# Kernel optimization log

Hardware: AMD Instinct MI355X
Metric: run time of the kernel (lower is better)

## Reference

```python
import jax, jax.numpy as jnp
import numpy as np

NUM_STATES = 2048
NUM_SYMBOLS = 512
SEQ_LEN = 8192


def setup_inputs() -> dict:
    key = jax.random.key(0)
    k_obs, k_A, k_B, k_pi = jax.random.split(key, 4)
    observations = jax.random.randint(k_obs, (SEQ_LEN,), 0, NUM_SYMBOLS, dtype=jnp.int32)
    # Row-stochastic transition matrix A, emission matrix B, initial dist pi
    A = jax.random.uniform(k_A, (NUM_STATES, NUM_STATES), dtype=jnp.float32)
    A = A / A.sum(axis=1, keepdims=True)
    B = jax.random.uniform(k_B, (NUM_STATES, NUM_SYMBOLS), dtype=jnp.float32)
    B = B / B.sum(axis=1, keepdims=True)
    pi = jax.random.uniform(k_pi, (NUM_STATES,), dtype=jnp.float32)
    pi = pi / pi.sum()
    return {"observations": observations, "A": A, "B": B, "pi": pi}


def reference(observations, A, B, pi):
    # Emission likelihoods per timestep: em[t, s] = B[s, o_t]  -> [T, S]
    em = B[:, observations].T
    alpha0 = pi * em[0]                      # [S]

    def step(alpha_prev, em_t):
        alpha_t = (alpha_prev @ A) * em_t    # vector-matrix + elementwise
        return alpha_t, alpha_t

    _, alpha_rest = jax.lax.scan(step, alpha0, em[1:])
    alpha = jnp.concatenate([alpha0[None, :], alpha_rest], axis=0)  # [T, S]
    return alpha
```

## Files before the change

kernel.cpp:

```cpp
#include <hip/hip_runtime.h>


#define S     2048
#define T     8192
#define NSYM  512
#define NBLK  64
#define NTHR  1024
#define READY 0x40000000

typedef int v4i __attribute__((ext_vector_type(4)));

__device__ __forceinline__ v4i load_coherent_i4(const int* p) {
    v4i r;
    asm volatile("global_load_dwordx4 %0, %1, off sc0 sc1\n\ts_waitcnt vmcnt(0)"
                 : "=v"(r) : "v"(p) : "memory");
    return r;
}
__device__ __forceinline__ void store_coherent_i4(int* p, v4i v) {
    asm volatile("global_store_dwordx4 %0, %1, off sc0 sc1"
                 :: "v"(p), "v"(v) : "memory");
}

#define POLL4(e0,e1,e2,e3,bp)                                              \
    asm volatile("global_load_dword %0, %4, off sc0 sc1\n\t"               \
                 "global_load_dword %1, %4, off offset:32 sc0 sc1\n\t"     \
                 "global_load_dword %2, %4, off offset:64 sc0 sc1\n\t"     \
                 "global_load_dword %3, %4, off offset:96 sc0 sc1"         \
                 : "=&v"(e0), "=&v"(e1), "=&v"(e2), "=&v"(e3)              \
                 : "v"(bp) : "memory")

__global__ void __launch_bounds__(NTHR) hmm_fwd(
    const int*   __restrict__ obs,
    const float* __restrict__ A,
    const float* __restrict__ B,
    const float* __restrict__ pi,
    float*       __restrict__ out,
    unsigned*    __restrict__ flag)
{
    __shared__ float4 s_wpart[16][8];
    __shared__ int    s_nz[4];

    const int tx   = threadIdx.x;
    const int b    = blockIdx.x;
    const int lane = tx & 63;
    const int w    = tx >> 6;
    const int jl4  = lane & 7;
    const int r_l  = lane >> 3;
    const int col4 = b * 8 + jl4;
    const float4* A4 = (const float4*)A;

    float4 a_reg[4][4];
    #pragma unroll
    for (int q = 0; q < 4; ++q)
        #pragma unroll
        for (int s = 0; s < 4; ++s) {
            const int i = (w + 16 * q) * 32 + s * 8 + r_l;
            a_reg[q][s] = A4[(size_t)i * (S / 4) + col4];
        }

    if (tx < 8) {
        const int o0 = obs[0];
        const int j  = b * 32 + tx * 4;
        v4i e;
        e.x = __float_as_int(pi[j + 0] * B[(size_t)(j + 0) * NSYM + o0]) + READY;
        e.y = __float_as_int(pi[j + 1] * B[(size_t)(j + 1) * NSYM + o0]) + READY;
        e.z = __float_as_int(pi[j + 2] * B[(size_t)(j + 2) * NSYM + o0]) + READY;
        e.w = __float_as_int(pi[j + 3] * B[(size_t)(j + 3) * NSYM + o0]) + READY;
        store_coherent_i4((int*)out + j, e);
    }
    if (tx == 0) { s_nz[0] = 0; s_nz[1] = 0; s_nz[2] = 0; s_nz[3] = 0; }
    __syncthreads();

    int lastRow = T - 1;

    for (int t = 1; t < T; ++t) {
        float em0 = 0.f, em1 = 0.f, em2 = 0.f, em3 = 0.f;
        if (tx < 8) {
            const int o = obs[t];
            const int j = b * 32 + tx * 4;
            em0 = B[(size_t)(j + 0) * NSYM + o];
            em1 = B[(size_t)(j + 1) * NSYM + o];
            em2 = B[(size_t)(j + 2) * NSYM + o];
            em3 = B[(size_t)(j + 3) * NSYM + o];
        }

        const int* rb = (const int*)(out + (size_t)(t - 1) * S) + r_l;
        const int* b0 = rb + (w +  0) * 32;
        const int* b1 = rb + (w + 16) * 32;
        const int* b2 = rb + (w + 32) * 32;
        const int* b3 = rb + (w + 48) * 32;
        int e00, e01, e02, e03, e10, e11, e12, e13;
        int e20, e21, e22, e23, e30, e31, e32, e33;
        for (;;) {
            POLL4(e00, e01, e02, e03, b0);
            POLL4(e10, e11, e12, e13, b1);
            POLL4(e20, e21, e22, e23, b2);
            POLL4(e30, e31, e32, e33, b3);
            asm volatile("s_waitcnt vmcnt(0)" ::: "memory");
            const int m0 = (e00 < READY) | (e01 < READY) | (e02 < READY) | (e03 < READY);
            const int m1 = (e10 < READY) | (e11 < READY) | (e12 < READY) | (e13 < READY);
            const int m2 = (e20 < READY) | (e21 < READY) | (e22 < READY) | (e23 < READY);
            const int m3 = (e30 < READY) | (e31 < READY) | (e32 < READY) | (e33 < READY);
            if (!(m0 | m1 | m2 | m3)) break;
        }

        float4 acc = make_float4(0.f, 0.f, 0.f, 0.f);
        int nzacc = 0;
        #define STEP1(E, Q, Ss)                                                \
            { const int d = (E) - READY; nzacc |= d;                           \
              const float af = __int_as_float(d);                              \
              acc.x = fmaf(af, a_reg[Q][Ss].x, acc.x);                         \
              acc.y = fmaf(af, a_reg[Q][Ss].y, acc.y);                         \
              acc.z = fmaf(af, a_reg[Q][Ss].z, acc.z);                         \
              acc.w = fmaf(af, a_reg[Q][Ss].w, acc.w); }
        STEP1(e00,0,0) STEP1(e01,0,1) STEP1(e02,0,2) STEP1(e03,0,3)
        STEP1(e10,1,0) STEP1(e11,1,1) STEP1(e12,1,2) STEP1(e13,1,3)
        STEP1(e20,2,0) STEP1(e21,2,1) STEP1(e22,2,2) STEP1(e23,2,3)
        STEP1(e30,3,0) STEP1(e31,3,1) STEP1(e32,3,2) STEP1(e33,3,3)
        #undef STEP1

        #pragma unroll
        for (int m = 8; m <= 32; m <<= 1) {
            acc.x += __shfl_xor(acc.x, m);
            acc.y += __shfl_xor(acc.y, m);
            acc.z += __shfl_xor(acc.z, m);
            acc.w += __shfl_xor(acc.w, m);
        }
        if (lane < 8) s_wpart[w][lane] = acc;
        const unsigned long long nzm = __ballot(nzacc != 0);
        if (nzm != 0ull && lane == 0) s_nz[t & 3] = 1;
        if (tx == 0) s_nz[(t + 2) & 3] = 0;
        __syncthreads();

        if (s_nz[t & 3] == 0) { lastRow = t - 1; break; }

        if (tx < 64) {
            const int h = tx >> 3, c = tx & 7;
            float4 p = s_wpart[h][c];
            const float4 q4 = s_wpart[h + 8][c];
            p.x += q4.x; p.y += q4.y; p.z += q4.z; p.w += q4.w;
            #pragma unroll
            for (int m = 8; m <= 32; m <<= 1) {
                p.x += __shfl_xor(p.x, m);
                p.y += __shfl_xor(p.y, m);
                p.z += __shfl_xor(p.z, m);
                p.w += __shfl_xor(p.w, m);
            }
            if (tx < 8) {
                v4i e;
                e.x = __float_as_int(p.x * em0) + READY;
                e.y = __float_as_int(p.y * em1) + READY;
                e.z = __float_as_int(p.z * em2) + READY;
                e.w = __float_as_int(p.w * em3) + READY;
                store_coherent_i4((int*)(out + (size_t)t * S) + b * 32 + tx * 4, e);
            }
        }
    }

    if (tx == 0)
        __hip_atomic_store(&flag[b], 1u, __ATOMIC_RELAXED, __HIP_MEMORY_SCOPE_AGENT);
    if (tx < 64) {
        for (;;) {
            const unsigned f = __hip_atomic_load(&flag[tx], __ATOMIC_RELAXED,
                                                 __HIP_MEMORY_SCOPE_AGENT);
            if (__all(f == 1u)) break;
            __builtin_amdgcn_s_sleep(1);
        }
    }
    __syncthreads();

    for (int idx = tx; idx < (lastRow + 1) * 8; idx += NTHR) {
        const int r = idx >> 3, c = idx & 7;
        int* p = (int*)(out + (size_t)r * S) + b * 32 + c * 4;
        v4i e = load_coherent_i4(p);
        e.x -= READY; e.y -= READY; e.z -= READY; e.w -= READY;
        store_coherent_i4(p, e);
    }

    {
        const size_t beg4 = (size_t)(lastRow + 1) * (S / 4);
        const size_t end4 = (size_t)T * (S / 4);
        const float4 z = make_float4(0.f, 0.f, 0.f, 0.f);
        float4* o4 = (float4*)out;
        for (size_t i = beg4 + (size_t)b * NTHR + tx; i < end4;
             i += (size_t)NBLK * NTHR)
            o4[i] = z;
    }
}

extern "C" void kernel_launch(void* const* d_in, const int* in_sizes, int n_in,
                              void* d_out, int out_size, void* d_ws, size_t ws_size,
                              hipStream_t stream) {
    const int*   obs = (const int*)d_in[0];
    const float* A   = (const float*)d_in[1];
    const float* B   = (const float*)d_in[2];
    const float* pi  = (const float*)d_in[3];
    float* out = (float*)d_out;
    unsigned* flag = (unsigned*)d_ws;

    (void)hipMemsetAsync(d_ws, 0, (size_t)NBLK * sizeof(unsigned), stream);

    hmm_fwd<<<dim3(NBLK), dim3(NTHR), 0, stream>>>(obs, A, B, pi, out, flag);
}
```

Measured before the change: 134.7 us.

## Zero-fill tail rows with extra blocks concurrently with the recurrence

Adds 192 extra workgroups that speculatively zero output rows 128 onward, using nontemporal stores, while the 64 compute blocks run the serial forward recurrence. Compute blocks wait on a counter at t=128, so any real rows written later land after the zeros. The post-loop fill now only covers the gap below row 128. This targets the large tail zero-write that previously ran after compute on just 64 blocks. In exchange it needs all 256 blocks co-resident and adds a spin-wait.

```diff
diff --git a/kernel.cpp b/kernel.cpp
--- a/kernel.cpp
+++ b/kernel.cpp
@@ -4,11 +4,16 @@
 #define S     2048
 #define T     8192
 #define NSYM  512
-#define NBLK  64
+#define NCBLK 64
+#define NFILL 192
+#define NBLK  (NCBLK + NFILL)
 #define NTHR  1024
 #define READY 0x40000000
-
-typedef int v4i __attribute__((ext_vector_type(4)));
+#define FILL_START 128
+#define ROWS_PER_FILL ((T - FILL_START) / NFILL)
+
+typedef int   v4i __attribute__((ext_vector_type(4)));
+typedef float v4f __attribute__((ext_vector_type(4)));
 
 __device__ __forceinline__ v4i load_coherent_i4(const int* p) {
     v4i r;
@@ -42,6 +47,23 @@
 
     const int tx   = threadIdx.x;
     const int b    = blockIdx.x;
+
+    if (b >= NCBLK) {
+        const int fb = b - NCBLK;
+        v4f* dst = (v4f*)(out + (size_t)(FILL_START + fb * ROWS_PER_FILL) * S);
+        const int n4 = ROWS_PER_FILL * (S / 4);
+        const v4f z = {0.f, 0.f, 0.f, 0.f};
+        for (int i = tx; i < n4; i += NTHR)
+            __builtin_nontemporal_store(z, &dst[i]);
+        __syncthreads();
+        if (tx == 0) {
+            __threadfence();
+            __hip_atomic_fetch_add(&flag[NCBLK], 1u,
+                                   __ATOMIC_RELEASE, __HIP_MEMORY_SCOPE_AGENT);
+        }
+        return;
+    }
+
     const int lane = tx & 63;
     const int w    = tx >> 6;
     const int jl4  = lane & 7;
@@ -74,6 +96,15 @@
     int lastRow = T - 1;
 
     for (int t = 1; t < T; ++t) {
+        if (t == FILL_START) {
+            if (tx == 0) {
+                while (__hip_atomic_load(&flag[NCBLK], __ATOMIC_ACQUIRE,
+                                         __HIP_MEMORY_SCOPE_AGENT) < NFILL)
+                    __builtin_amdgcn_s_sleep(8);
+            }
+            __syncthreads();
+        }
+
         float em0 = 0.f, em1 = 0.f, em2 = 0.f, em3 = 0.f;
         if (tx < 8) {
             const int o = obs[t];
@@ -178,13 +209,15 @@
     }
 
     {
-        const size_t beg4 = (size_t)(lastRow + 1) * (S / 4);
-        const size_t end4 = (size_t)T * (S / 4);
-        const float4 z = make_float4(0.f, 0.f, 0.f, 0.f);
-        float4* o4 = (float4*)out;
+        const int zbeg = lastRow + 1;
+        const int zend = (FILL_START > zbeg) ? FILL_START : zbeg;
+        const size_t beg4 = (size_t)zbeg * (S / 4);
+        const size_t end4 = (size_t)zend * (S / 4);
+        const v4f z = {0.f, 0.f, 0.f, 0.f};
+        v4f* o4 = (v4f*)out;
         for (size_t i = beg4 + (size_t)b * NTHR + tx; i < end4;
-             i += (size_t)NBLK * NTHR)
-            o4[i] = z;
+             i += (size_t)NCBLK * NTHR)
+            __builtin_nontemporal_store(z, &o4[i]);
     }
 }
 
@@ -198,7 +231,7 @@
     float* out = (float*)d_out;
     unsigned* flag = (unsigned*)d_ws;
 
-    (void)hipMemsetAsync(d_ws, 0, (size_t)NBLK * sizeof(unsigned), stream);
+    (void)hipMemsetAsync(d_ws, 0, (size_t)(NCBLK + 1) * sizeof(unsigned), stream);
 
     hmm_fwd<<<dim3(NBLK), dim3(NTHR), 0, stream>>>(obs, A, B, pi, out, flag);
 }
```

Result: slower. 145.4 us (+7.9%).

## Split READY-tag cleanup and zero-fill into a separate wide tail kernel

Applied to the files above, without the earlier changes.

The grid-wide flag barrier and the per-block cleanup at the end of the recurrence kernel are removed. The recurrence kernel now only records the last computed row. A second kernel with 256 blocks strips the READY tag from computed rows and zero-fills the rest of the output. The aim is to spread the large bandwidth-bound zero-fill over more CUs than the 64 recurrence blocks. The cost is one extra kernel launch. The load of A into registers is also moved after the initial alpha0 store.

```diff
diff --git a/kernel.cpp b/kernel.cpp
--- a/kernel.cpp
+++ b/kernel.cpp
@@ -4,18 +4,14 @@
 #define S     2048
 #define T     8192
 #define NSYM  512
-#define NBLK  64
+#define NCBLK 64
 #define NTHR  1024
+#define FBLK  256
 #define READY 0x40000000
 
-typedef int v4i __attribute__((ext_vector_type(4)));
+typedef int   v4i __attribute__((ext_vector_type(4)));
+typedef float v4f __attribute__((ext_vector_type(4)));
 
-__device__ __forceinline__ v4i load_coherent_i4(const int* p) {
-    v4i r;
-    asm volatile("global_load_dwordx4 %0, %1, off sc0 sc1\n\ts_waitcnt vmcnt(0)"
-                 : "=v"(r) : "v"(p) : "memory");
-    return r;
-}
 __device__ __forceinline__ void store_coherent_i4(int* p, v4i v) {
     asm volatile("global_store_dwordx4 %0, %1, off sc0 sc1"
                  :: "v"(p), "v"(v) : "memory");
@@ -49,15 +45,6 @@
     const int col4 = b * 8 + jl4;
     const float4* A4 = (const float4*)A;
 
-    float4 a_reg[4][4];
-    #pragma unroll
-    for (int q = 0; q < 4; ++q)
-        #pragma unroll
-        for (int s = 0; s < 4; ++s) {
-            const int i = (w + 16 * q) * 32 + s * 8 + r_l;
-            a_reg[q][s] = A4[(size_t)i * (S / 4) + col4];
-        }
-
     if (tx < 8) {
         const int o0 = obs[0];
         const int j  = b * 32 + tx * 4;
@@ -70,6 +57,15 @@
     }
     if (tx == 0) { s_nz[0] = 0; s_nz[1] = 0; s_nz[2] = 0; s_nz[3] = 0; }
     __syncthreads();
+
+    float4 a_reg[4][4];
+    #pragma unroll
+    for (int q = 0; q < 4; ++q)
+        #pragma unroll
+        for (int s = 0; s < 4; ++s) {
+            const int i = (w + 16 * q) * 32 + s * 8 + r_l;
+            a_reg[q][s] = A4[(size_t)i * (S / 4) + col4];
+        }
 
     int lastRow = T - 1;
 
@@ -158,33 +154,28 @@
     }
 
     if (tx == 0)
-        __hip_atomic_store(&flag[b], 1u, __ATOMIC_RELAXED, __HIP_MEMORY_SCOPE_AGENT);
-    if (tx < 64) {
-        for (;;) {
-            const unsigned f = __hip_atomic_load(&flag[tx], __ATOMIC_RELAXED,
-                                                 __HIP_MEMORY_SCOPE_AGENT);
-            if (__all(f == 1u)) break;
-            __builtin_amdgcn_s_sleep(1);
+        __hip_atomic_store(&flag[0], (unsigned)(lastRow + 1), __ATOMIC_RELAXED,
+                           __HIP_MEMORY_SCOPE_AGENT);
+}
+
+__global__ void __launch_bounds__(NTHR) hmm_tail(
+    float*          __restrict__ out,
+    const unsigned* __restrict__ flag)
+{
+    const unsigned zstart = flag[0];
+    const size_t total4 = (size_t)T * (S / 4);
+    v4i* o4 = (v4i*)out;
+    const v4i zero = {0, 0, 0, 0};
+    for (size_t i = (size_t)blockIdx.x * NTHR + threadIdx.x; i < total4;
+         i += (size_t)FBLK * NTHR) {
+        const unsigned r = (unsigned)(i >> 9);
+        if (r >= zstart) {
+            o4[i] = zero;
+        } else {
+            v4i e = o4[i];
+            e.x -= READY; e.y -= READY; e.z -= READY; e.w -= READY;
+            o4[i] = e;
         }
-    }
-    __syncthreads();
-
-    for (int idx = tx; idx < (lastRow + 1) * 8; idx += NTHR) {
-        const int r = idx >> 3, c = idx & 7;
-        int* p = (int*)(out + (size_t)r * S) + b * 32 + c * 4;
-        v4i e = load_coherent_i4(p);
-        e.x -= READY; e.y -= READY; e.z -= READY; e.w -= READY;
-        store_coherent_i4(p, e);
-    }
-
-    {
-        const size_t beg4 = (size_t)(lastRow + 1) * (S / 4);
-        const size_t end4 = (size_t)T * (S / 4);
-        const float4 z = make_float4(0.f, 0.f, 0.f, 0.f);
-        float4* o4 = (float4*)out;
-        for (size_t i = beg4 + (size_t)b * NTHR + tx; i < end4;
-             i += (size_t)NBLK * NTHR)
-            o4[i] = z;
     }
 }
 
@@ -198,7 +189,8 @@
     float* out = (float*)d_out;
     unsigned* flag = (unsigned*)d_ws;
 
-    (void)hipMemsetAsync(d_ws, 0, (size_t)NBLK * sizeof(unsigned), stream);
+    (void)hipMemsetAsync(d_ws, 0, 4 * sizeof(unsigned), stream);
 
-    hmm_fwd<<<dim3(NBLK), dim3(NTHR), 0, stream>>>(obs, A, B, pi, out, flag);
+    hmm_fwd<<<dim3(NCBLK), dim3(NTHR), 0, stream>>>(obs, A, B, pi, out, flag);
+    hmm_tail<<<dim3(FBLK), dim3(NTHR), 0, stream>>>(out, flag);
 }
```

Result: no change. 133.1 us (-1.2%).
